# Performance work log

Hardware: AMD Instinct MI355X
Metric: run time of the kernel (lower is better)

The kernel has to match this reference:

```python
import jax, jax.numpy as jnp
import numpy as np

D_MODEL, D_MLP, D_HEAD, N_HEADS, SEQ, BATCH = 1024, 4096, 64, 16, 2048, 2


def setup_inputs() -> dict:
    key = jax.random.key(0)
    ks = jax.random.split(key, 7)
    s = 1.0 / np.sqrt(D_MODEL)
    return {
        "x": jax.random.normal(ks[0], (BATCH, SEQ, D_MODEL), jnp.float32),
        "W_K": jax.random.normal(ks[1], (N_HEADS, D_HEAD, D_MODEL), jnp.float32) * s,
        "W_Q": jax.random.normal(ks[2], (N_HEADS, D_HEAD, D_MODEL), jnp.float32) * s,
        "W_V": jax.random.normal(ks[3], (N_HEADS, D_HEAD, D_MODEL), jnp.float32) * s,
        "W_O": jax.random.normal(ks[4], (D_MODEL, N_HEADS * D_HEAD), jnp.float32) * s,
        "W_in": jax.random.normal(ks[5], (D_MLP, D_MODEL), jnp.float32) * s,
        "b_in": jnp.zeros((D_MLP,), jnp.float32),
        "W_out": jax.random.normal(ks[6], (D_MODEL, D_MLP), jnp.float32) * s,
        "b_out": jnp.zeros((D_MODEL,), jnp.float32),
    }


def _block(x, W_K, W_Q, W_V, W_O, W_in, b_in, W_out, b_out):
    S = x.shape[-2]
    # attention
    k = jnp.einsum('ihd,bpd->biph', W_K, x)
    q = jnp.einsum('ihd,bpd->biph', W_Q, x)
    v = jnp.einsum('ihd,bpd->biph', W_V, x)
    scores = jnp.einsum('biph,biqh->biqp', k, q)  # [B,H,S(query q),S(key p)]
    causal = jnp.tril(jnp.ones((S, S), x.dtype))
    masked = jnp.tril(scores) - 1e10 * (1.0 - causal)
    attn = jax.nn.softmax(masked / np.sqrt(D_HEAD), axis=-1)
    z = jnp.einsum('biph,biqp->biqh', v, attn)  # [B,H,S,d_head]
    z_flat = jnp.transpose(z, (0, 2, 1, 3)).reshape(x.shape[0], S, -1)  # b q (i h)
    attn_out = jnp.einsum('df,bqf->bqd', W_O, z_flat)
    x = x + attn_out
    # MLP
    h = jax.nn.relu(jnp.einsum('md,bpd->bpm', W_in, x) + b_in)
    x = x + jnp.einsum('dm,bpm->bpd', W_out, h) + b_out
    return x


def reference(x, W_K, W_Q, W_V, W_O, W_in, b_in, W_out, b_out):
    return _block(x, W_K, W_Q, W_V, W_O, W_in, b_in, W_out, b_out)
```

## Files before the change

kernel.cpp:

```cpp
#include <hip/hip_runtime.h>

typedef unsigned short u16;
typedef __bf16 bf16x8 __attribute__((ext_vector_type(8)));
typedef float f32x4 __attribute__((ext_vector_type(4)));
typedef u16 u16x8 __attribute__((ext_vector_type(8), may_alias));
typedef u16 u16x4 __attribute__((ext_vector_type(4), may_alias));
typedef unsigned int u32x4 __attribute__((ext_vector_type(4)));

#define D_MODEL 1024
#define D_MLP   4096
#define D_HEAD  64
#define N_HEADS 16
#define SEQ     2048
#define BATCH   2
#define BS      (BATCH * SEQ)
#define QKV_N   3072
#define QSCALE  0.18033688011112042f

__device__ __forceinline__ u16 f2b(float f) {
  unsigned u = __builtin_bit_cast(unsigned, f);
  u += 0x7fffu + ((u >> 16) & 1u);
  return (u16)(u >> 16);
}

__device__ __forceinline__ unsigned cvtpk_bf16(float lo, float hi) {
  unsigned r;
  asm("v_cvt_pk_bf16_f32 %0, %1, %2" : "=v"(r) : "v"(lo), "v"(hi));
  return r;
}

__device__ __forceinline__ void gload_lds16(const u16* g, u16* l) {
  __builtin_amdgcn_global_load_lds(
      (const __attribute__((address_space(1))) unsigned int*)g,
      (__attribute__((address_space(3))) unsigned int*)l, 16, 0, 0);
}

__global__ __launch_bounds__(256) void cvt_all(
    const float* __restrict__ x,  const float* __restrict__ wq,
    const float* __restrict__ wk, const float* __restrict__ wv,
    const float* __restrict__ wo, const float* __restrict__ wi,
    const float* __restrict__ wu,
    u16* __restrict__ xb, u16* __restrict__ wqkv, u16* __restrict__ wo_b,
    u16* __restrict__ win_b, u16* __restrict__ wout_b)
{
  const int i = blockIdx.x * 256 + threadIdx.x;
  const float* src; u16* dst; int j;
  if (i < 1048576)      { src = x;  dst = xb;              j = i; }
  else if (i < 1310720) { src = wq; dst = wqkv;            j = i - 1048576; }
  else if (i < 1572864) { src = wk; dst = wqkv + 1048576;  j = i - 1310720; }
  else if (i < 1835008) { src = wv; dst = wqkv + 2097152;  j = i - 1572864; }
  else if (i < 2097152) { src = wo; dst = wo_b;            j = i - 1835008; }
  else if (i < 3145728) { src = wi; dst = win_b;           j = i - 2097152; }
  else                  { src = wu; dst = wout_b;          j = i - 3145728; }
  float4 v = ((const float4*)src)[j];
  u16x4 o;
  o[0] = f2b(v.x); o[1] = f2b(v.y); o[2] = f2b(v.z); o[3] = f2b(v.w);
  ((u16x4*)dst)[j] = o;
}

template<int MODE, int BM>
__global__ __launch_bounds__(256) void gemm_bt(
    const u16* __restrict__ A, const u16* __restrict__ Bw,
    int M, int N, int K,
    u16* __restrict__ outb, float* __restrict__ outf,
    const float* __restrict__ resid, const float* __restrict__ bias,
    u16* __restrict__ vtp, int gx)
{
  constexpr int MI = BM / 32;
  __shared__ u16 Asm_[BM * 64];
  __shared__ u16 Bsm_[128 * 64];
  const int t = threadIdx.x;
  const int lane = t & 63;
  const int l15 = lane & 15, l4 = lane >> 4;
  const int w = t >> 6;
  const int wr = w >> 1, wc = w & 1;

  int bx, by;
  if constexpr (BM == 64) {
    bx = blockIdx.x & 7;
    by = blockIdx.x >> 3;
  } else {
    const int xcd = blockIdx.x & 7;
    const int local = blockIdx.x >> 3;
    const int rw = gx >> 2;
    const int rx = xcd & 3, ry = xcd >> 2;
    const int c = local >> 4, r0 = local & 15;
    bx = rx * rw + c;
    by = ry * 16 + r0;
  }
  int z = 0;
  if (MODE == 3) { z = bx >> 3; bx &= 7; }
  const int m0 = by * BM;
  const int n0 = bx * 128;
  const int kb = (MODE == 3) ? z * (K >> 1) : 0;
  const int ke = (MODE == 3) ? kb + (K >> 1) : K;

  f32x4 acc[MI][4] = {};

  for (int k0 = kb; k0 < ke; k0 += 64) {
    __syncthreads();
#pragma unroll
    for (int i = 0; i < 4; ++i) {
      int s = i * 256 + t;
      int row = s >> 3;
      int sl = s & 7;
      int gc = ((sl ^ (row & 7)) << 3);
      const u16* gb = Bw + (size_t)(n0 + row) * K + (k0 + gc);
      u16* lb = Bsm_ + (i * 256 + (t & ~63)) * 8;
      if (BM == 128 || i < 2) {
        const u16* ga = A + (size_t)(m0 + row) * K + (k0 + gc);
        u16* la = Asm_ + (i * 256 + (t & ~63)) * 8;
        gload_lds16(ga, la);
      }
      gload_lds16(gb, lb);
    }
    asm volatile("s_waitcnt vmcnt(0)" ::: "memory");
    __syncthreads();
#pragma unroll
    for (int kk = 0; kk < 2; ++kk) {
      bf16x8 af[MI], bfr[4];
#pragma unroll
      for (int mi = 0; mi < MI; ++mi) {
        int row = wr * (BM / 2) + mi * 16 + l15;
        int sl2 = (kk * 4 + l4) ^ (row & 7);
        u16x8 ua = *(const u16x8*)(Asm_ + row * 64 + sl2 * 8);
        af[mi] = __builtin_bit_cast(bf16x8, ua);
      }
#pragma unroll
      for (int ni = 0; ni < 4; ++ni) {
        int row = wc * 64 + ni * 16 + l15;
        int sl2 = (kk * 4 + l4) ^ (row & 7);
        u16x8 ub = *(const u16x8*)(Bsm_ + row * 64 + sl2 * 8);
        bfr[ni] = __builtin_bit_cast(bf16x8, ub);
      }
#pragma unroll
      for (int mi = 0; mi < MI; ++mi)
#pragma unroll
        for (int ni = 0; ni < 4; ++ni)
          acc[mi][ni] = __builtin_amdgcn_mfma_f32_16x16x32_bf16(af[mi], bfr[ni], acc[mi][ni], 0, 0, 0);
    }
  }

#pragma unroll
  for (int mi = 0; mi < MI; ++mi) {
    int rowb = m0 + wr * (BM / 2) + mi * 16 + l4 * 4;
#pragma unroll
    for (int ni = 0; ni < 4; ++ni) {
      int col = n0 + wc * 64 + ni * 16 + l15;
#pragma unroll
      for (int r = 0; r < 4; ++r) {
        float v = acc[mi][ni][r];
        int row = rowb + r;
        if (MODE == 0) {
          if (col < 2048) {
            float o = (col < 1024) ? v * QSCALE : v;
            outb[((size_t)row << 11) + col] = f2b(o);
          } else {
            int c2 = col - 2048;
            size_t vi = (((size_t)((row >> 11) * 1024 + c2)) << 11) + (row & (SEQ - 1));
            vtp[vi] = f2b(v);
          }
        } else if (MODE == 3) {
          outf[(size_t)z * M * N + (size_t)row * N + col] = v;
        } else {
          size_t idx = (size_t)row * N + col;
          if (MODE == 1) {
            float o = v + resid[idx];
            outf[idx] = o;
            outb[idx] = f2b(o);
          } else {
            float o = v + bias[col];
            o = o > 0.f ? o : 0.f;
            outb[idx] = f2b(o);
          }
        }
      }
    }
  }
}

__global__ __launch_bounds__(256) void reduce2_kernel(const float* __restrict__ part,
                                                      const float* __restrict__ resid,
                                                      const float* __restrict__ bias,
                                                      float* __restrict__ out) {
  const int i = blockIdx.x * 256 + threadIdx.x;
  float4 a = ((const float4*)part)[i];
  float4 b = ((const float4*)(part + (size_t)BS * D_MODEL))[i];
  float4 r = ((const float4*)resid)[i];
  float4 bi = ((const float4*)bias)[i & 255];
  float4 o;
  o.x = a.x + b.x + r.x + bi.x;
  o.y = a.y + b.y + r.y + bi.y;
  o.z = a.z + b.z + r.z + bi.z;
  o.w = a.w + b.w + r.w + bi.w;
  ((float4*)out)[i] = o;
}

__global__ __launch_bounds__(256) void attn_kernel(const u16* __restrict__ qk,
                                                   const u16* __restrict__ vT,
                                                   u16* __restrict__ zb)
{
  __shared__ u16 Kl[2][128 * 64];
  __shared__ u16 Vl[2][64 * 136];
  const int t = threadIdx.x;
  const int w = t >> 6;
  const int lane = t & 63;
  const int l15 = lane & 15, l4 = lane >> 4;
  const int blk = blockIdx.x;
  const int bh = blk & 31;
  const int qb = 15 - (blk >> 5);
  const int b = bh >> 4, h = bh & 15;
  const int q0w = qb * 128 + w * 32;
  const int ttmax = qb;

  bf16x8 qf[2][2];
#pragma unroll
  for (int s = 0; s < 2; ++s) {
    const u16* qp = qk + (((size_t)(b * SEQ + q0w + s * 16 + l15)) << 11) + h * 64 + l4 * 8;
    qf[s][0] = __builtin_bit_cast(bf16x8, *(const u16x8*)(qp));
    qf[s][1] = __builtin_bit_cast(bf16x8, *(const u16x8*)(qp + 32));
  }

  const int srow = t >> 3;
  const int sgc = ((t & 7) ^ (srow & 7)) * 8;
  const u16* kgbase = qk + (((size_t)(b * SEQ + srow)) << 11) + 1024 + h * 64 + sgc;
  u16* kldst = &Kl[0][0] + (t & ~63) * 8;
  const int vd2 = t >> 2, q4 = t & 3;
  const u16* vgbase = vT + (((size_t)(bh * 64 + vd2)) << 11);

  f32x4 zacc[2][4] = {};
  float m_run[2] = {-1e30f, -1e30f}, l_run[2] = {0.f, 0.f};

  auto stageK = [&](int buf, int tt) {
    const u16* kg = kgbase + ((size_t)tt << 18);
    u16* kld = kldst + buf * (128 * 64);
#pragma unroll
    for (int i = 0; i < 4; ++i)
      gload_lds16(kg + ((size_t)i << 16), kld + i * 2048);
  };

  auto compute = [&](int buf, int tt) {
    const bool last = (tt == ttmax);
    f32x4 sf[2][8] = {};
    __builtin_amdgcn_s_setprio(1);
#pragma unroll
    for (int ks = 0; ks < 8; ++ks) {
      const int row = ks * 16 + l15;
#pragma unroll
      for (int kc = 0; kc < 2; ++kc) {
        const int slot = (kc * 4 + l4) ^ (row & 7);
        bf16x8 kf = __builtin_bit_cast(bf16x8,
            *(const u16x8*)&Kl[buf][row * 64 + slot * 8]);
        sf[0][ks] = __builtin_amdgcn_mfma_f32_16x16x32_bf16(kf, qf[0][kc], sf[0][ks], 0, 0, 0);
        sf[1][ks] = __builtin_amdgcn_mfma_f32_16x16x32_bf16(kf, qf[1][kc], sf[1][ks], 0, 0, 0);
      }
    }
    __builtin_amdgcn_s_setprio(0);

    if (last) {
      const int pb = tt * 128 + l4 * 4;
#pragma unroll
      for (int s = 0; s < 2; ++s) {
        const int qq = q0w + s * 16 + l15;
#pragma unroll
        for (int ks = 0; ks < 8; ++ks)
#pragma unroll
          for (int r = 0; r < 4; ++r)
            sf[s][ks][r] = (pb + ks * 16 + r <= qq) ? sf[s][ks][r] : -1e30f;
      }
    }

    float mn[2], sc_[2];
#pragma unroll
    for (int s = 0; s < 2; ++s) {
      float mk[8];
#pragma unroll
      for (int ks = 0; ks < 8; ++ks)
        mk[ks] = fmaxf(fmaxf(sf[s][ks][0], sf[s][ks][1]), fmaxf(sf[s][ks][2], sf[s][ks][3]));
      float mt = fmaxf(fmaxf(fmaxf(mk[0], mk[1]), fmaxf(mk[2], mk[3])),
                       fmaxf(fmaxf(mk[4], mk[5]), fmaxf(mk[6], mk[7])));
      mt = fmaxf(mt, __shfl_xor(mt, 16));
      mt = fmaxf(mt, __shfl_xor(mt, 32));
      mn[s] = fmaxf(m_run[s], mt);
      sc_[s] = __builtin_amdgcn_exp2f(m_run[s] - mn[s]);
      m_run[s] = mn[s];
    }
#pragma unroll
    for (int s = 0; s < 2; ++s) {
      float rs = 0.f;
#pragma unroll
      for (int ks = 0; ks < 8; ++ks)
#pragma unroll
        for (int r = 0; r < 4; ++r) {
          sf[s][ks][r] = __builtin_amdgcn_exp2f(sf[s][ks][r] - mn[s]);
          rs += sf[s][ks][r];
        }
      rs += __shfl_xor(rs, 16);
      rs += __shfl_xor(rs, 32);
      l_run[s] = l_run[s] * sc_[s] + rs;
#pragma unroll
      for (int dn = 0; dn < 4; ++dn)
#pragma unroll
        for (int r = 0; r < 4; ++r) zacc[s][dn][r] *= sc_[s];
    }

    bf16x8 pa[2][4];
#pragma unroll
    for (int s = 0; s < 2; ++s)
#pragma unroll
      for (int g = 0; g < 4; ++g) {
        u32x4 pu;
        pu[0] = cvtpk_bf16(sf[s][2 * g][0], sf[s][2 * g][1]);
        pu[1] = cvtpk_bf16(sf[s][2 * g][2], sf[s][2 * g][3]);
        pu[2] = cvtpk_bf16(sf[s][2 * g + 1][0], sf[s][2 * g + 1][1]);
        pu[3] = cvtpk_bf16(sf[s][2 * g + 1][2], sf[s][2 * g + 1][3]);
        pa[s][g] = __builtin_bit_cast(bf16x8, pu);
      }

    __builtin_amdgcn_s_setprio(1);
#pragma unroll
    for (int g = 0; g < 4; ++g)
#pragma unroll
      for (int dn = 0; dn < 4; ++dn) {
        bf16x8 vfr = __builtin_bit_cast(bf16x8,
            *(const u16x8*)&Vl[buf][(dn * 16 + l15) * 136 + g * 32 + l4 * 8]);
        zacc[0][dn] = __builtin_amdgcn_mfma_f32_16x16x32_bf16(vfr, pa[0][g], zacc[0][dn], 0, 0, 0);
        zacc[1][dn] = __builtin_amdgcn_mfma_f32_16x16x32_bf16(vfr, pa[1][g], zacc[1][dn], 0, 0, 0);
      }
    __builtin_amdgcn_s_setprio(0);
  };

  stageK(0, 0);
  {
#pragma unroll
    for (int g = 0; g < 4; ++g) {
      const u16* vg = vgbase + g * 32 + q4 * 4;
      u16x4 lo = *(const u16x4*)(vg);
      u16x4 hi = *(const u16x4*)(vg + 16);
      *(u16x8*)&Vl[0][vd2 * 136 + g * 32 + q4 * 8] =
          __builtin_shufflevector(lo, hi, 0, 1, 2, 3, 4, 5, 6, 7);
    }
  }
  asm volatile("s_waitcnt vmcnt(0)" ::: "memory");
  __syncthreads();

  int cur = 0;
  for (int tt = 0; tt <= ttmax; ++tt) {
    const bool more = tt < ttmax;
    u16x4 lo[4], hi[4];
    if (more) {
      stageK(cur ^ 1, tt + 1);
#pragma unroll
      for (int g = 0; g < 4; ++g) {
        const u16* vg = vgbase + (tt + 1) * 128 + g * 32 + q4 * 4;
        lo[g] = *(const u16x4*)(vg);
        hi[g] = *(const u16x4*)(vg + 16);
      }
    }
    compute(cur, tt);
    if (more) {
#pragma unroll
      for (int g = 0; g < 4; ++g)
        *(u16x8*)&Vl[cur ^ 1][vd2 * 136 + g * 32 + q4 * 8] =
            __builtin_shufflevector(lo[g], hi[g], 0, 1, 2, 3, 4, 5, 6, 7);
    }
    asm volatile("s_waitcnt vmcnt(0)" ::: "memory");
    __syncthreads();
    cur ^= 1;
  }

#pragma unroll
  for (int s = 0; s < 2; ++s) {
    const float inv = 1.f / l_run[s];
    const size_t rowoff = ((size_t)(b * SEQ + q0w + s * 16 + l15)) * D_MODEL + h * 64 + l4 * 4;
#pragma unroll
    for (int dn = 0; dn < 4; ++dn) {
      u16x4 o;
#pragma unroll
      for (int r = 0; r < 4; ++r) o[r] = f2b(zacc[s][dn][r] * inv);
      *(u16x4*)(zb + rowoff + dn * 16) = o;
    }
  }
}

extern "C" void kernel_launch(void* const* d_in, const int* in_sizes, int n_in,
                              void* d_out, int out_size, void* d_ws, size_t ws_size,
                              hipStream_t stream) {
  const float* x     = (const float*)d_in[0];
  const float* W_K   = (const float*)d_in[1];
  const float* W_Q   = (const float*)d_in[2];
  const float* W_V   = (const float*)d_in[3];
  const float* W_O   = (const float*)d_in[4];
  const float* W_in  = (const float*)d_in[5];
  const float* b_in  = (const float*)d_in[6];
  const float* W_out = (const float*)d_in[7];
  const float* b_out = (const float*)d_in[8];
  float* out = (float*)d_out;

  char* p = (char*)d_ws;
  float* x1f  = (float*)p;         p += (size_t)BS * D_MODEL * 4;
  u16* hb     = (u16*)p;           p += (size_t)BS * D_MLP * 2;
  u16* wout_b = (u16*)p;           p += (size_t)D_MODEL * D_MLP * 2;
  u16* xb     = (u16*)p;           p += (size_t)BS * D_MODEL * 2;
  u16* wqkv   = (u16*)p;           p += (size_t)QKV_N * D_MODEL * 2;
  u16* wo_b   = (u16*)p;           p += (size_t)D_MODEL * D_MODEL * 2;
  u16* win_b  = (u16*)p;           p += (size_t)D_MLP * D_MODEL * 2;
  u16* qk     = (u16*)p;           p += (size_t)BS * 2048 * 2;
  u16* vt     = (u16*)p;           p += (size_t)BATCH * 1024 * SEQ * 2;
  u16* zb     = (u16*)p;           p += (size_t)BS * D_MODEL * 2;
  u16* x1b    = (u16*)p;           p += (size_t)BS * D_MODEL * 2;
  float* part = (float*)xb;

  cvt_all<<<dim3(16384), 256, 0, stream>>>(
      x, W_Q, W_K, W_V, W_O, W_in, W_out, xb, wqkv, wo_b, win_b, wout_b);

  gemm_bt<0, 128><<<dim3(24 * 32), 256, 0, stream>>>(
      xb, wqkv, BS, QKV_N, D_MODEL, qk, nullptr, nullptr, nullptr, vt, 24);

  attn_kernel<<<dim3(512), 256, 0, stream>>>(qk, vt, zb);

  gemm_bt<1, 64><<<dim3(512), 256, 0, stream>>>(
      zb, wo_b, BS, D_MODEL, D_MODEL, x1b, x1f, x, nullptr, nullptr, 8);

  gemm_bt<2, 128><<<dim3(32 * 32), 256, 0, stream>>>(
      x1b, win_b, BS, D_MLP, D_MODEL, hb, nullptr, nullptr, b_in, nullptr, 32);

  gemm_bt<3, 128><<<dim3(16 * 32), 256, 0, stream>>>(
      hb, wout_b, BS, D_MODEL, D_MLP, nullptr, part, nullptr, nullptr, nullptr, 16);

  reduce2_kernel<<<dim3(BS * D_MODEL / 4 / 256), 256, 0, stream>>>(part, x1f, b_out, out);
}
```

Measured before the change: 237.5 us.

## Use 256x256-tile double-buffered GEMM kernel for QKV and MLP-in projections

Adds a 512-thread GEMM kernel with 256x256 output tiles, double-buffered LDS staging through direct global-to-LDS loads, and an XOR swizzle. The QKV projection and the MLP up-projection now use it in place of the 128-tile kernel. The larger tiles raise arithmetic intensity and cut redundant global loads, and the two-stage buffer overlaps loads with MFMA work. In exchange, grids get small (192 and 256 blocks on a large-CU part), LDS use is high (128KB per block), and register pressure from the 8x4 accumulator tiles could limit occupancy.

```diff
diff --git a/kernel.cpp b/kernel.cpp
--- a/kernel.cpp
+++ b/kernel.cpp
@@ -58,6 +58,107 @@
   ((u16x4*)dst)[j] = o;
 }
 
+template<int MODE>
+__global__ __launch_bounds__(512) void gemm256(
+    const u16* __restrict__ A, const u16* __restrict__ Bw,
+    int M, int N, int K,
+    u16* __restrict__ outb, const float* __restrict__ bias,
+    u16* __restrict__ vtp, int gx)
+{
+  __shared__ u16 Al[2][256 * 64];
+  __shared__ u16 Bl[2][256 * 64];
+  const int t = threadIdx.x;
+  const int lane = t & 63;
+  const int l15 = lane & 15, l4 = lane >> 4;
+  const int wid = t >> 6;
+  const int wm = wid >> 2, wn = wid & 3;
+
+  const int g4 = blockIdx.x >> 2;
+  const int bx = g4 % gx;
+  const int by = (g4 / gx) * 4 + (blockIdx.x & 3);
+  const int m0 = by * 256, n0 = bx * 256;
+  const int nk = K >> 6;
+
+  auto stage = [&](int k, int buf) {
+#pragma unroll
+    for (int i = 0; i < 4; ++i) {
+      int s = i * 512 + t;
+      int row = s >> 3;
+      int gc = ((s & 7) ^ (row & 7)) << 3;
+      const u16* ga = A + (size_t)(m0 + row) * K + (k << 6) + gc;
+      const u16* gb = Bw + (size_t)(n0 + row) * K + (k << 6) + gc;
+      gload_lds16(ga, &Al[buf][(s & ~63) * 8]);
+      gload_lds16(gb, &Bl[buf][(s & ~63) * 8]);
+    }
+  };
+
+  f32x4 acc[8][4] = {};
+
+  stage(0, 0);
+  stage(1, 1);
+  asm volatile("s_waitcnt vmcnt(8)" ::: "memory");
+  __syncthreads();
+
+  for (int k = 0; k < nk; ++k) {
+    const int buf = k & 1;
+#pragma unroll
+    for (int kk = 0; kk < 2; ++kk) {
+      bf16x8 bfr[4];
+#pragma unroll
+      for (int ni = 0; ni < 4; ++ni) {
+        int row = wn * 64 + ni * 16 + l15;
+        int slot = (kk * 4 + l4) ^ (row & 7);
+        bfr[ni] = __builtin_bit_cast(bf16x8, *(const u16x8*)&Bl[buf][row * 64 + slot * 8]);
+      }
+#pragma unroll
+      for (int mi = 0; mi < 8; ++mi) {
+        int row = wm * 128 + mi * 16 + l15;
+        int slot = (kk * 4 + l4) ^ (row & 7);
+        bf16x8 af = __builtin_bit_cast(bf16x8, *(const u16x8*)&Al[buf][row * 64 + slot * 8]);
+#pragma unroll
+        for (int ni = 0; ni < 4; ++ni)
+          acc[mi][ni] = __builtin_amdgcn_mfma_f32_16x16x32_bf16(af, bfr[ni], acc[mi][ni], 0, 0, 0);
+      }
+    }
+    __syncthreads();
+    if (k + 2 < nk) {
+      stage(k + 2, buf);
+      asm volatile("s_waitcnt vmcnt(8)" ::: "memory");
+    } else {
+      asm volatile("s_waitcnt vmcnt(0)" ::: "memory");
+    }
+    __syncthreads();
+  }
+
+#pragma unroll
+  for (int mi = 0; mi < 8; ++mi) {
+    int rowb = m0 + wm * 128 + mi * 16 + l4 * 4;
+#pragma unroll
+    for (int ni = 0; ni < 4; ++ni) {
+      int col = n0 + wn * 64 + ni * 16 + l15;
+#pragma unroll
+      for (int r = 0; r < 4; ++r) {
+        float v = acc[mi][ni][r];
+        int row = rowb + r;
+        if (MODE == 0) {
+          if (col < 2048) {
+            float o = (col < 1024) ? v * QSCALE : v;
+            outb[((size_t)row << 11) + col] = f2b(o);
+          } else {
+            int c2 = col - 2048;
+            size_t vi = (((size_t)((row >> 11) * 1024 + c2)) << 11) + (row & (SEQ - 1));
+            vtp[vi] = f2b(v);
+          }
+        } else {
+          float o = v + bias[col];
+          o = o > 0.f ? o : 0.f;
+          outb[(size_t)row * N + col] = f2b(o);
+        }
+      }
+    }
+  }
+}
+
 template<int MODE, int BM>
 __global__ __launch_bounds__(256) void gemm_bt(
     const u16* __restrict__ A, const u16* __restrict__ Bw,
@@ -151,28 +252,13 @@
       for (int r = 0; r < 4; ++r) {
         float v = acc[mi][ni][r];
         int row = rowb + r;
-        if (MODE == 0) {
-          if (col < 2048) {
-            float o = (col < 1024) ? v * QSCALE : v;
-            outb[((size_t)row << 11) + col] = f2b(o);
-          } else {
-            int c2 = col - 2048;
-            size_t vi = (((size_t)((row >> 11) * 1024 + c2)) << 11) + (row & (SEQ - 1));
-            vtp[vi] = f2b(v);
-          }
-        } else if (MODE == 3) {
-          outf[(size_t)z * M * N + (size_t)row * N + col] = v;
+        size_t idx = (size_t)row * N + col;
+        if (MODE == 3) {
+          outf[(size_t)z * M * N + idx] = v;
         } else {
-          size_t idx = (size_t)row * N + col;
-          if (MODE == 1) {
-            float o = v + resid[idx];
-            outf[idx] = o;
-            outb[idx] = f2b(o);
-          } else {
-            float o = v + bias[col];
-            o = o > 0.f ? o : 0.f;
-            outb[idx] = f2b(o);
-          }
+          float o = v + resid[idx];
+          outf[idx] = o;
+          outb[idx] = f2b(o);
         }
       }
     }
@@ -414,16 +500,16 @@
   cvt_all<<<dim3(16384), 256, 0, stream>>>(
       x, W_Q, W_K, W_V, W_O, W_in, W_out, xb, wqkv, wo_b, win_b, wout_b);
 
-  gemm_bt<0, 128><<<dim3(24 * 32), 256, 0, stream>>>(
-      xb, wqkv, BS, QKV_N, D_MODEL, qk, nullptr, nullptr, nullptr, vt, 24);
+  gemm256<0><<<dim3(192), 512, 0, stream>>>(
+      xb, wqkv, BS, QKV_N, D_MODEL, qk, nullptr, vt, 12);
 
   attn_kernel<<<dim3(512), 256, 0, stream>>>(qk, vt, zb);
 
   gemm_bt<1, 64><<<dim3(512), 256, 0, stream>>>(
       zb, wo_b, BS, D_MODEL, D_MODEL, x1b, x1f, x, nullptr, nullptr, 8);
 
-  gemm_bt<2, 128><<<dim3(32 * 32), 256, 0, stream>>>(
-      x1b, win_b, BS, D_MLP, D_MODEL, hb, nullptr, nullptr, b_in, nullptr, 32);
+  gemm256<2><<<dim3(256), 512, 0, stream>>>(
+      x1b, win_b, BS, D_MLP, D_MODEL, hb, b_in, nullptr, 16);
 
   gemm_bt<3, 128><<<dim3(16 * 32), 256, 0, stream>>>(
       hb, wout_b, BS, D_MODEL, D_MLP, nullptr, part, nullptr, nullptr, nullptr, 16);
```

New measurement: 238.1 us. Within noise of the previous version (+0.3%).
